# Kernel optimization log

Hardware: AMD Instinct MI355X
Metric: run time of the kernel (lower is better)

Reference implementation:

```python
import jax, jax.numpy as jnp
import numpy as np

N_S = 50000
N_T = 50000
E = 800000
D_IN = 128
D_OUT = 128


def setup_inputs() -> dict:
    key = jax.random.key(0)
    k1, k2, k3, k4 = jax.random.split(key, 4)
    edge_index = jax.random.randint(k1, (2, E), 0, N_S, dtype=jnp.int64)
    x_s = jax.random.normal(k2, (N_S, D_IN), dtype=jnp.float32)
    x_t = jax.random.normal(k3, (N_T, D_IN), dtype=jnp.float32)
    # glorot-ish linear weight of GCNConv (bias=False)
    W = jax.random.normal(k4, (D_IN, D_OUT), dtype=jnp.float32) * (1.0 / np.sqrt(D_IN))
    return {"edge_index": edge_index, "x_s": x_s, "x_t": x_t, "W": W}


def reference(edge_index, x_s, x_t, W):
    N_s = x_s.shape[0]
    N_t = x_t.shape[0]
    N = N_s + N_t
    # dropout p=0.0 -> identity; concat bipartite features
    x = jnp.concatenate([x_s, x_t], axis=0)  # [N, d_in]
    row = edge_index[0]
    col = edge_index[1] + N_s  # module shifts target indices in-place
    # GCNConv: add self-loops with weight 1
    loops = jnp.arange(N, dtype=row.dtype)
    row_f = jnp.concatenate([row, loops])
    col_f = jnp.concatenate([col, loops])
    w = jnp.ones(row_f.shape[0], dtype=x.dtype)
    # symmetric degree normalization: deg computed on target (col)
    deg = jax.ops.segment_sum(w, col_f, num_segments=N)
    deg_inv_sqrt = jnp.where(deg > 0, jax.lax.rsqrt(deg), 0.0)
    norm = deg_inv_sqrt[row_f] * deg_inv_sqrt[col_f]  # [E+N]
    # linear transform then normalized scatter-add aggregation
    h = x @ W  # [N, d_out]
    msg = h[row_f] * norm[:, None]  # gather + scale, [E+N, d_out]
    out = jax.ops.segment_sum(msg, col_f, num_segments=N)  # scatter-add
    out = jax.nn.relu(out)
    return out[:N_s], out[N_s:]
```

## Files before the change

### kernel.cpp

```cpp
#include <hip/hip_runtime.h>
#include <hip/hip_bf16.h>
#include <math.h>

#define NSRC 50000
#define NTGT 50000
#define NTOT 100000
#define NEDGE 800000
#define DIM 128
#define WPAD 136

#define NBUCK 782
#define BCAP 1536
#define EPT 8
#define EPB2 2048
#define PBLK2 391
#define GEMM_GRID 1563
#define FGRID (PBLK2 + GEMM_GRID)

typedef __attribute__((ext_vector_type(8))) short short8;
typedef __attribute__((ext_vector_type(4))) float float4v;

union U8 { short8 s; uint4 u; };

__device__ __forceinline__ unsigned short f2bf(float f) {
    unsigned u = __float_as_uint(f);
    unsigned r = (u + 0x7FFFu + ((u >> 16) & 1u)) >> 16;
    return (unsigned short)r;
}
__device__ __forceinline__ float bf2f(unsigned us) {
    return __uint_as_float(us << 16);
}
__device__ __forceinline__ unsigned pkbf(float lo, float hi) {
    __hip_bfloat162 b = __float22bfloat162_rn(make_float2(lo, hi));
    return *(unsigned*)&b;
}

__global__ void k_prep(const float* __restrict__ W, unsigned short* __restrict__ Wt,
                       int* __restrict__ bcnt) {
    int i = blockIdx.x * blockDim.x + threadIdx.x;
    if (i < NBUCK) bcnt[i] = 0;
    if (i < DIM * DIM) {
        int k = i >> 7, n = i & 127;
        Wt[n * DIM + k] = f2bf(W[i]);
    }
}

__global__ __launch_bounds__(256) void k_front(const int* __restrict__ row,
                                               const int* __restrict__ col,
                                               int* __restrict__ bcnt,
                                               unsigned* __restrict__ part,
                                               const float* __restrict__ xsrc,
                                               const float* __restrict__ xtgt,
                                               const unsigned short* __restrict__ Wt,
                                               unsigned short* __restrict__ h,
                                               float* __restrict__ out) {
    __shared__ union SM {
        struct { int hist[NBUCK]; int runbase[NBUCK]; int cur[NBUCK]; } p;
        unsigned short Bs[128 * WPAD];
    } sm;

    const int tid = threadIdx.x;

    if (blockIdx.x < PBLK2) {
        for (int i = tid; i < NBUCK; i += 256) sm.p.hist[i] = 0;
        __syncthreads();

        int e0 = blockIdx.x * EPB2 + tid * EPT;
        bool valid = (e0 + EPT <= NEDGE);
        int c[EPT], r[EPT];
        if (valid) {
            *(int4*)&c[0] = *(const int4*)(col + e0);
            *(int4*)&c[4] = *(const int4*)(col + e0 + 4);
            *(int4*)&r[0] = *(const int4*)(row + e0);
            *(int4*)&r[4] = *(const int4*)(row + e0 + 4);
#pragma unroll
            for (int i = 0; i < EPT; ++i) atomicAdd(&sm.p.hist[c[i] >> 6], 1);
        }
        __syncthreads();
        for (int i = tid; i < NBUCK; i += 256) {
            sm.p.runbase[i] = atomicAdd(&bcnt[i], sm.p.hist[i]);
            sm.p.cur[i] = 0;
        }
        __syncthreads();
        if (valid) {
#pragma unroll
            for (int i = 0; i < EPT; ++i) {
                int q = c[i] >> 6;
                int pos = sm.p.runbase[q] + atomicAdd(&sm.p.cur[q], 1);
                part[q * BCAP + pos] = (unsigned)r[i] | ((unsigned)(c[i] & 63) << 16);
            }
        }
        return;
    }

    const int gb = blockIdx.x - PBLK2;

    for (int idx = tid; idx < 2048; idx += 256) {
        int n = idx >> 4, c8 = idx & 15;
        *(uint4*)&sm.Bs[n * WPAD + c8 * 8] = *(const uint4*)(Wt + n * DIM + c8 * 8);
    }

    const int wave = tid >> 6, lane = tid & 63;
    const int nl = lane & 15, quad = lane >> 4;

    int node = gb * 64 + wave * 16 + nl;
    int mc = (node < NTOT) ? node : (NTOT - 1);
    const float* xrow = (mc < NSRC) ? (xsrc + (size_t)mc * DIM)
                                    : (xtgt + (size_t)(mc - NSRC) * DIM);
    float4 a[8];
#pragma unroll
    for (int s = 0; s < 4; ++s) {
        a[2 * s]     = *(const float4*)(xrow + s * 32 + quad * 8);
        a[2 * s + 1] = *(const float4*)(xrow + s * 32 + quad * 8 + 4);
    }
    __syncthreads();

    float4v acc[8];
#pragma unroll
    for (int t = 0; t < 8; ++t) acc[t] = (float4v){0.f, 0.f, 0.f, 0.f};

#pragma unroll
    for (int s = 0; s < 4; ++s) {
        U8 af;
        af.u.x = pkbf(a[2 * s].x, a[2 * s].y);
        af.u.y = pkbf(a[2 * s].z, a[2 * s].w);
        af.u.z = pkbf(a[2 * s + 1].x, a[2 * s + 1].y);
        af.u.w = pkbf(a[2 * s + 1].z, a[2 * s + 1].w);
#pragma unroll
        for (int t = 0; t < 8; ++t) {
            short8 bf = *(const short8*)&sm.Bs[(t * 16 + nl) * WPAD + s * 32 + quad * 8];
            acc[t] = __builtin_amdgcn_mfma_f32_16x16x32_bf16(bf, af.s, acc[t], 0, 0, 0);
        }
    }

    if (node < NTOT) {
        unsigned short* hp = h + (size_t)node * DIM + quad * 4;
        float* op = out + (size_t)node * DIM + quad * 4;
        bool isrc = (node < NSRC);
#pragma unroll
        for (int t = 0; t < 8; ++t) {
            uint2 p;
            p.x = pkbf(acc[t][0], acc[t][1]);
            p.y = pkbf(acc[t][2], acc[t][3]);
            *(uint2*)(hp + t * 16) = p;
            if (isrc) {
                float4 o;
                o.x = fmaxf(acc[t][0], 0.f);
                o.y = fmaxf(acc[t][1], 0.f);
                o.z = fmaxf(acc[t][2], 0.f);
                o.w = fmaxf(acc[t][3], 0.f);
                *(float4*)(op + t * 16) = o;
            }
        }
    }
}

__global__ __launch_bounds__(256) void k_bucket(const int* __restrict__ bcnt,
                                                const unsigned* __restrict__ part,
                                                unsigned short* __restrict__ csr,
                                                int* __restrict__ tstart,
                                                int* __restrict__ tcnt) {
    __shared__ unsigned ebuf[BCAP];
    __shared__ unsigned short srt[BCAP];
    __shared__ int hist[64], bufA[64], bufB[64], cur[64];

    int q = blockIdx.x, tid = threadIdx.x;
    int n = bcnt[q];
    int base = q * BCAP;

    if (tid < 64) hist[tid] = 0;
    __syncthreads();
    for (int i = tid; i < n; i += 256) {
        unsigned p = part[base + i];
        ebuf[i] = p;
        atomicAdd(&hist[p >> 16], 1);
    }
    __syncthreads();

    if (tid < 64) bufA[tid] = hist[tid];
    int* src = bufA; int* dst = bufB;
    for (int d = 1; d < 64; d <<= 1) {
        __syncthreads();
        if (tid < 64) dst[tid] = src[tid] + ((tid >= d) ? src[tid - d] : 0);
        int* t = src; src = dst; dst = t;
    }
    __syncthreads();
    if (tid < 64) {
        int excl = src[tid] - hist[tid];
        cur[tid] = excl;
        int c = q * 64 + tid;
        if (c < NTGT) {
            tstart[c] = base + excl;
            tcnt[c] = hist[tid];
        }
    }
    __syncthreads();

    for (int i = tid; i < n; i += 256) {
        unsigned p = ebuf[i];
        int pos = atomicAdd(&cur[p >> 16], 1);
        srt[pos] = (unsigned short)(p & 0xffffu);
    }
    __syncthreads();
    int m = (n + 1) >> 1;
    unsigned* dst32 = (unsigned*)(csr + base);
    for (int i = tid; i < m; i += 256) dst32[i] = ((unsigned*)srt)[i];
}

__global__ __launch_bounds__(256) void k_agg(const int* __restrict__ tstart,
                                             const int* __restrict__ tcnt,
                                             const unsigned short* __restrict__ csr,
                                             const unsigned short* __restrict__ h,
                                             float* __restrict__ out) {
    int w = threadIdx.x >> 6;
    int lane = threadIdx.x & 63;
    int c = blockIdx.x * 4 + w;
    if (c >= NTGT) return;

    int n = tcnt[c];
    int s0 = tstart[c];
    int q = lane >> 4;
    int ql = lane & 15;

    float acc[8];
#pragma unroll
    for (int i = 0; i < 8; ++i) acc[i] = 0.f;

    int j = 0;
    while (j < n) {
        int nb = (n - j < 64) ? (n - j) : 64;
        int v = (lane < nb) ? (int)csr[s0 + j + lane] : 0;
        int n4 = nb & ~3;
        int kk = 0;
#pragma unroll 4
        for (; kk < n4; kk += 4) {
            int r = __shfl(v, kk + q, 64);
            uint4 d = *(const uint4*)(h + (size_t)r * DIM + ql * 8);
            acc[0] += bf2f(d.x & 0xffff); acc[1] += bf2f(d.x >> 16);
            acc[2] += bf2f(d.y & 0xffff); acc[3] += bf2f(d.y >> 16);
            acc[4] += bf2f(d.z & 0xffff); acc[5] += bf2f(d.z >> 16);
            acc[6] += bf2f(d.w & 0xffff); acc[7] += bf2f(d.w >> 16);
        }
        int rem = nb - kk;
        if (rem) {
            int qq = (q < rem) ? q : 0;
            int r = __shfl(v, kk + qq, 64);
            if (q < rem) {
                uint4 d = *(const uint4*)(h + (size_t)r * DIM + ql * 8);
                acc[0] += bf2f(d.x & 0xffff); acc[1] += bf2f(d.x >> 16);
                acc[2] += bf2f(d.y & 0xffff); acc[3] += bf2f(d.y >> 16);
                acc[4] += bf2f(d.z & 0xffff); acc[5] += bf2f(d.z >> 16);
                acc[6] += bf2f(d.w & 0xffff); acc[7] += bf2f(d.w >> 16);
            }
        }
        j += nb;
    }

#pragma unroll
    for (int i = 0; i < 8; ++i) {
        acc[i] += __shfl_xor(acc[i], 16, 64);
        acc[i] += __shfl_xor(acc[i], 32, 64);
    }

    if (q == 0) {
        float di = rsqrtf(1.0f + (float)n);
        float dd = di * di;
        uint4 dh = *(const uint4*)(h + (size_t)(NSRC + c) * DIM + ql * 8);
        float4 o0, o1;
        o0.x = fmaxf(di * acc[0] + dd * bf2f(dh.x & 0xffff), 0.f);
        o0.y = fmaxf(di * acc[1] + dd * bf2f(dh.x >> 16), 0.f);
        o0.z = fmaxf(di * acc[2] + dd * bf2f(dh.y & 0xffff), 0.f);
        o0.w = fmaxf(di * acc[3] + dd * bf2f(dh.y >> 16), 0.f);
        o1.x = fmaxf(di * acc[4] + dd * bf2f(dh.z & 0xffff), 0.f);
        o1.y = fmaxf(di * acc[5] + dd * bf2f(dh.z >> 16), 0.f);
        o1.z = fmaxf(di * acc[6] + dd * bf2f(dh.w & 0xffff), 0.f);
        o1.w = fmaxf(di * acc[7] + dd * bf2f(dh.w >> 16), 0.f);
        float* op = out + (size_t)(NSRC + c) * DIM + ql * 8;
        *(float4*)op = o0;
        *(float4*)(op + 4) = o1;
    }
}

extern "C" void kernel_launch(void* const* d_in, const int* in_sizes, int n_in,
                              void* d_out, int out_size, void* d_ws, size_t ws_size,
                              hipStream_t stream) {
    const int* ei     = (const int*)d_in[0];
    const float* xsrc = (const float*)d_in[1];
    const float* xtgt = (const float*)d_in[2];
    const float* W    = (const float*)d_in[3];
    float* out = (float*)d_out;

    const int* row = ei;
    const int* col = ei + NEDGE;

    char* ws = (char*)d_ws;
    unsigned short* h  = (unsigned short*)ws;  ws += (size_t)NTOT * DIM * 2;
    unsigned short* Wt = (unsigned short*)ws;  ws += DIM * DIM * 2;
    unsigned* part = (unsigned*)ws;            ws += (size_t)NBUCK * BCAP * 4;
    unsigned short* csr = (unsigned short*)ws; ws += (size_t)NBUCK * BCAP * 2;
    int* bcnt   = (int*)ws;                    ws += NBUCK * 4;
    int* tstart = (int*)ws;                    ws += NTGT * 4;
    int* tcnt   = (int*)ws;                    ws += NTGT * 4;

    k_prep<<<(DIM * DIM + 255) / 256, 256, 0, stream>>>(W, Wt, bcnt);
    k_front<<<FGRID, 256, 0, stream>>>(row, col, bcnt, part, xsrc, xtgt, Wt, h, out);
    k_bucket<<<NBUCK, 256, 0, stream>>>(bcnt, part, csr, tstart, tcnt);
    k_agg<<<(NTGT + 3) / 4, 256, 0, stream>>>(tstart, tcnt, csr, h, out);
}
```

Baseline: 172.5 us.

## Fuse bucket sort with aggregation and interleave partition blocks among GEMM blocks

Merges the per-bucket sort and the per-target aggregation into a single kernel that reads neighbor indices from shared memory, removing the CSR/tstart/tcnt global writes and one launch. Partition blocks are interleaved every fifth block with GEMM blocks so both kinds of work run concurrently. Bucket counters are padded to separate cache lines, and W is prepacked in MFMA fragment order so LDS loads become linear. The fused kernel has only 782 blocks each handling 64 targets serially per wave, reducing parallelism and latency hiding for the gather.

```diff
diff --git a/kernel.cpp b/kernel.cpp
--- a/kernel.cpp
+++ b/kernel.cpp
@@ -7,10 +7,10 @@
 #define NTOT 100000
 #define NEDGE 800000
 #define DIM 128
-#define WPAD 136
 
 #define NBUCK 782
 #define BCAP 1536
+#define BPAD 16
 #define EPT 8
 #define EPB2 2048
 #define PBLK2 391
@@ -35,14 +35,15 @@
     return *(unsigned*)&b;
 }
 
-__global__ void k_prep(const float* __restrict__ W, unsigned short* __restrict__ Wt,
-                       int* __restrict__ bcnt) {
-    int i = blockIdx.x * blockDim.x + threadIdx.x;
-    if (i < NBUCK) bcnt[i] = 0;
-    if (i < DIM * DIM) {
-        int k = i >> 7, n = i & 127;
-        Wt[n * DIM + k] = f2bf(W[i]);
-    }
+__global__ __launch_bounds__(256) void k_prep(const float* __restrict__ W,
+                                              unsigned short* __restrict__ Wt,
+                                              int* __restrict__ bcnt) {
+    int i = blockIdx.x * 256 + threadIdx.x;
+    if (i < NBUCK * BPAD) bcnt[i] = 0;
+    int j = i & 7, lane = (i >> 3) & 63, ts = i >> 9;
+    int t = ts >> 2, s = ts & 3;
+    int nl = lane & 15, qd = lane >> 4;
+    Wt[i] = f2bf(W[(s * 32 + qd * 8 + j) * DIM + (t * 16 + nl)]);
 }
 
 __global__ __launch_bounds__(256) void k_front(const int* __restrict__ row,
@@ -56,16 +57,17 @@
                                                float* __restrict__ out) {
     __shared__ union SM {
         struct { int hist[NBUCK]; int runbase[NBUCK]; int cur[NBUCK]; } p;
-        unsigned short Bs[128 * WPAD];
+        unsigned short Bs[DIM * DIM];
     } sm;
 
     const int tid = threadIdx.x;
-
-    if (blockIdx.x < PBLK2) {
+    const int bid = blockIdx.x;
+
+    if (bid % 5 == 0) {
         for (int i = tid; i < NBUCK; i += 256) sm.p.hist[i] = 0;
         __syncthreads();
 
-        int e0 = blockIdx.x * EPB2 + tid * EPT;
+        int e0 = (bid / 5) * EPB2 + tid * EPT;
         bool valid = (e0 + EPT <= NEDGE);
         int c[EPT], r[EPT];
         if (valid) {
@@ -78,7 +80,7 @@
         }
         __syncthreads();
         for (int i = tid; i < NBUCK; i += 256) {
-            sm.p.runbase[i] = atomicAdd(&bcnt[i], sm.p.hist[i]);
+            sm.p.runbase[i] = atomicAdd(&bcnt[i * BPAD], sm.p.hist[i]);
             sm.p.cur[i] = 0;
         }
         __syncthreads();
@@ -93,12 +95,10 @@
         return;
     }
 
-    const int gb = blockIdx.x - PBLK2;
-
-    for (int idx = tid; idx < 2048; idx += 256) {
-        int n = idx >> 4, c8 = idx & 15;
-        *(uint4*)&sm.Bs[n * WPAD + c8 * 8] = *(const uint4*)(Wt + n * DIM + c8 * 8);
-    }
+    const int gb = bid - bid / 5 - 1;
+
+    for (int idx = tid; idx < 2048; idx += 256)
+        ((uint4*)sm.Bs)[idx] = ((const uint4*)Wt)[idx];
 
     const int wave = tid >> 6, lane = tid & 63;
     const int nl = lane & 15, quad = lane >> 4;
@@ -128,7 +128,7 @@
         af.u.w = pkbf(a[2 * s + 1].z, a[2 * s + 1].w);
 #pragma unroll
         for (int t = 0; t < 8; ++t) {
-            short8 bf = *(const short8*)&sm.Bs[(t * 16 + nl) * WPAD + s * 32 + quad * 8];
+            short8 bf = *(const short8*)&sm.Bs[((t * 4 + s) * 64 + lane) * 8];
             acc[t] = __builtin_amdgcn_mfma_f32_16x16x32_bf16(bf, af.s, acc[t], 0, 0, 0);
         }
     }
@@ -155,17 +155,16 @@
     }
 }
 
-__global__ __launch_bounds__(256) void k_bucket(const int* __restrict__ bcnt,
-                                                const unsigned* __restrict__ part,
-                                                unsigned short* __restrict__ csr,
-                                                int* __restrict__ tstart,
-                                                int* __restrict__ tcnt) {
+__global__ __launch_bounds__(256) void k_back(const int* __restrict__ bcnt,
+                                              const unsigned* __restrict__ part,
+                                              const unsigned short* __restrict__ h,
+                                              float* __restrict__ out) {
     __shared__ unsigned ebuf[BCAP];
     __shared__ unsigned short srt[BCAP];
-    __shared__ int hist[64], bufA[64], bufB[64], cur[64];
+    __shared__ int hist[64], bufA[64], bufB[64], cur[64], st[64];
 
     int q = blockIdx.x, tid = threadIdx.x;
-    int n = bcnt[q];
+    int n = bcnt[q * BPAD];
     int base = q * BCAP;
 
     if (tid < 64) hist[tid] = 0;
@@ -182,102 +181,78 @@
     for (int d = 1; d < 64; d <<= 1) {
         __syncthreads();
         if (tid < 64) dst[tid] = src[tid] + ((tid >= d) ? src[tid - d] : 0);
-        int* t = src; src = dst; dst = t;
+        int* tp = src; src = dst; dst = tp;
     }
     __syncthreads();
     if (tid < 64) {
         int excl = src[tid] - hist[tid];
         cur[tid] = excl;
-        int c = q * 64 + tid;
-        if (c < NTGT) {
-            tstart[c] = base + excl;
-            tcnt[c] = hist[tid];
-        }
-    }
-    __syncthreads();
-
+        st[tid] = excl;
+    }
+    __syncthreads();
     for (int i = tid; i < n; i += 256) {
         unsigned p = ebuf[i];
         int pos = atomicAdd(&cur[p >> 16], 1);
         srt[pos] = (unsigned short)(p & 0xffffu);
     }
     __syncthreads();
-    int m = (n + 1) >> 1;
-    unsigned* dst32 = (unsigned*)(csr + base);
-    for (int i = tid; i < m; i += 256) dst32[i] = ((unsigned*)srt)[i];
-}
-
-__global__ __launch_bounds__(256) void k_agg(const int* __restrict__ tstart,
-                                             const int* __restrict__ tcnt,
-                                             const unsigned short* __restrict__ csr,
-                                             const unsigned short* __restrict__ h,
-                                             float* __restrict__ out) {
-    int w = threadIdx.x >> 6;
-    int lane = threadIdx.x & 63;
-    int c = blockIdx.x * 4 + w;
-    if (c >= NTGT) return;
-
-    int n = tcnt[c];
-    int s0 = tstart[c];
-    int q = lane >> 4;
-    int ql = lane & 15;
-
-    float acc[8];
-#pragma unroll
-    for (int i = 0; i < 8; ++i) acc[i] = 0.f;
-
-    int j = 0;
-    while (j < n) {
-        int nb = (n - j < 64) ? (n - j) : 64;
-        int v = (lane < nb) ? (int)csr[s0 + j + lane] : 0;
-        int n4 = nb & ~3;
+
+    int w = tid >> 6, lane = tid & 63;
+    int qd = lane >> 4, ql = lane & 15;
+
+    for (int t = 0; t < 16; ++t) {
+        int cl = w * 16 + t;
+        int c = q * 64 + cl;
+        if (c >= NTGT) break;
+        int nn = hist[cl];
+        int s0 = st[cl];
+
+        float acc[8];
+#pragma unroll
+        for (int i = 0; i < 8; ++i) acc[i] = 0.f;
+
         int kk = 0;
 #pragma unroll 4
-        for (; kk < n4; kk += 4) {
-            int r = __shfl(v, kk + q, 64);
+        for (; kk + 4 <= nn; kk += 4) {
+            int r = (int)srt[s0 + kk + qd];
             uint4 d = *(const uint4*)(h + (size_t)r * DIM + ql * 8);
             acc[0] += bf2f(d.x & 0xffff); acc[1] += bf2f(d.x >> 16);
             acc[2] += bf2f(d.y & 0xffff); acc[3] += bf2f(d.y >> 16);
             acc[4] += bf2f(d.z & 0xffff); acc[5] += bf2f(d.z >> 16);
             acc[6] += bf2f(d.w & 0xffff); acc[7] += bf2f(d.w >> 16);
         }
-        int rem = nb - kk;
-        if (rem) {
-            int qq = (q < rem) ? q : 0;
-            int r = __shfl(v, kk + qq, 64);
-            if (q < rem) {
-                uint4 d = *(const uint4*)(h + (size_t)r * DIM + ql * 8);
-                acc[0] += bf2f(d.x & 0xffff); acc[1] += bf2f(d.x >> 16);
-                acc[2] += bf2f(d.y & 0xffff); acc[3] += bf2f(d.y >> 16);
-                acc[4] += bf2f(d.z & 0xffff); acc[5] += bf2f(d.z >> 16);
-                acc[6] += bf2f(d.w & 0xffff); acc[7] += bf2f(d.w >> 16);
-            }
-        }
-        j += nb;
-    }
-
-#pragma unroll
-    for (int i = 0; i < 8; ++i) {
-        acc[i] += __shfl_xor(acc[i], 16, 64);
-        acc[i] += __shfl_xor(acc[i], 32, 64);
-    }
-
-    if (q == 0) {
-        float di = rsqrtf(1.0f + (float)n);
-        float dd = di * di;
-        uint4 dh = *(const uint4*)(h + (size_t)(NSRC + c) * DIM + ql * 8);
-        float4 o0, o1;
-        o0.x = fmaxf(di * acc[0] + dd * bf2f(dh.x & 0xffff), 0.f);
-        o0.y = fmaxf(di * acc[1] + dd * bf2f(dh.x >> 16), 0.f);
-        o0.z = fmaxf(di * acc[2] + dd * bf2f(dh.y & 0xffff), 0.f);
-        o0.w = fmaxf(di * acc[3] + dd * bf2f(dh.y >> 16), 0.f);
-        o1.x = fmaxf(di * acc[4] + dd * bf2f(dh.z & 0xffff), 0.f);
-        o1.y = fmaxf(di * acc[5] + dd * bf2f(dh.z >> 16), 0.f);
-        o1.z = fmaxf(di * acc[6] + dd * bf2f(dh.w & 0xffff), 0.f);
-        o1.w = fmaxf(di * acc[7] + dd * bf2f(dh.w >> 16), 0.f);
-        float* op = out + (size_t)(NSRC + c) * DIM + ql * 8;
-        *(float4*)op = o0;
-        *(float4*)(op + 4) = o1;
+        if (qd < nn - kk) {
+            int r = (int)srt[s0 + kk + qd];
+            uint4 d = *(const uint4*)(h + (size_t)r * DIM + ql * 8);
+            acc[0] += bf2f(d.x & 0xffff); acc[1] += bf2f(d.x >> 16);
+            acc[2] += bf2f(d.y & 0xffff); acc[3] += bf2f(d.y >> 16);
+            acc[4] += bf2f(d.z & 0xffff); acc[5] += bf2f(d.z >> 16);
+            acc[6] += bf2f(d.w & 0xffff); acc[7] += bf2f(d.w >> 16);
+        }
+
+#pragma unroll
+        for (int i = 0; i < 8; ++i) {
+            acc[i] += __shfl_xor(acc[i], 16, 64);
+            acc[i] += __shfl_xor(acc[i], 32, 64);
+        }
+
+        if (qd == 0) {
+            float di = rsqrtf(1.0f + (float)nn);
+            float dd = di * di;
+            uint4 dh = *(const uint4*)(h + (size_t)(NSRC + c) * DIM + ql * 8);
+            float4 o0, o1;
+            o0.x = fmaxf(di * acc[0] + dd * bf2f(dh.x & 0xffff), 0.f);
+            o0.y = fmaxf(di * acc[1] + dd * bf2f(dh.x >> 16), 0.f);
+            o0.z = fmaxf(di * acc[2] + dd * bf2f(dh.y & 0xffff), 0.f);
+            o0.w = fmaxf(di * acc[3] + dd * bf2f(dh.y >> 16), 0.f);
+            o1.x = fmaxf(di * acc[4] + dd * bf2f(dh.z & 0xffff), 0.f);
+            o1.y = fmaxf(di * acc[5] + dd * bf2f(dh.z >> 16), 0.f);
+            o1.z = fmaxf(di * acc[6] + dd * bf2f(dh.w & 0xffff), 0.f);
+            o1.w = fmaxf(di * acc[7] + dd * bf2f(dh.w >> 16), 0.f);
+            float* op = out + (size_t)(NSRC + c) * DIM + ql * 8;
+            *(float4*)op = o0;
+            *(float4*)(op + 4) = o1;
+        }
     }
 }
 
@@ -297,13 +272,9 @@
     unsigned short* h  = (unsigned short*)ws;  ws += (size_t)NTOT * DIM * 2;
     unsigned short* Wt = (unsigned short*)ws;  ws += DIM * DIM * 2;
     unsigned* part = (unsigned*)ws;            ws += (size_t)NBUCK * BCAP * 4;
-    unsigned short* csr = (unsigned short*)ws; ws += (size_t)NBUCK * BCAP * 2;
-    int* bcnt   = (int*)ws;                    ws += NBUCK * 4;
-    int* tstart = (int*)ws;                    ws += NTGT * 4;
-    int* tcnt   = (int*)ws;                    ws += NTGT * 4;
-
-    k_prep<<<(DIM * DIM + 255) / 256, 256, 0, stream>>>(W, Wt, bcnt);
+    int* bcnt = (int*)ws;                      ws += NBUCK * BPAD * 4;
+
+    k_prep<<<64, 256, 0, stream>>>(W, Wt, bcnt);
     k_front<<<FGRID, 256, 0, stream>>>(row, col, bcnt, part, xsrc, xtgt, Wt, h, out);
-    k_bucket<<<NBUCK, 256, 0, stream>>>(bcnt, part, csr, tstart, tcnt);
-    k_agg<<<(NTGT + 3) / 4, 256, 0, stream>>>(tstart, tcnt, csr, h, out);
-}
+    k_back<<<NBUCK, 256, 0, stream>>>(bcnt, part, h, out);
+}
```

Result: faster. 166.9 us (-3.2%).
